# Kernel tuning notes

Hardware: AMD Instinct MI355X
Metric: run time of the kernel (lower is better)

## Reference

```python
import jax, jax.numpy as jnp
import numpy as np
import math

B, N, F = 4, 4096, 64
NEG_SLOPE = 0.01


def _leaky_relu(x):
    return jnp.where(x >= 0, x, NEG_SLOPE * x)


def setup_inputs() -> dict:
    key = jax.random.key(0)
    k1, k2, k3, k4, k5 = jax.random.split(key, 5)
    Q = jax.random.normal(k1, (B, N, F, 2), dtype=jnp.float32)
    K = jax.random.normal(k2, (B, N, F, 2), dtype=jnp.float32)
    V = jax.random.normal(k3, (B, N, F, 2), dtype=jnp.float32)
    W_att = jax.random.normal(k4, (F, F), dtype=jnp.float32) / math.sqrt(F)
    b_att = jax.random.normal(k5, (F,), dtype=jnp.float32) * 0.01
    return {"Q": Q, "K": K, "V": V, "W_att": W_att, "b_att": b_att}


def reference(Q, K, V, W_att, b_att):
    # Split complex components: last axis is (real, imag)
    Qr, Qi = Q[..., 0], Q[..., 1]
    Kr, Ki = K[..., 0], K[..., 1]
    Vr, Vi = V[..., 0], V[..., 1]

    n = Q.shape[1]
    scale = 1.0 / math.sqrt(n)  # num_nodes == N

    # Complex scores = Q @ K^T (no conjugation, as in torch einsum on complex)
    sr = (jnp.einsum('bik,bjk->bij', Qr, Kr) - jnp.einsum('bik,bjk->bij', Qi, Ki)) * scale
    si = (jnp.einsum('bik,bjk->bij', Qr, Ki) + jnp.einsum('bik,bjk->bij', Qi, Kr)) * scale

    # Causal mask: positions j > i are masked out (contribute zero weight)
    causal = jnp.tril(jnp.ones((n, n), dtype=bool))  # [N, N], True = keep
    wr = jnp.where(causal, _leaky_relu(sr), 0.0)
    wi = jnp.where(causal, _leaky_relu(si), 0.0)

    # Attention-weighted values (real weights with real V, imag with imag V)
    out_r = jnp.einsum('bij,bjf->bif', wr, Vr)
    out_i = jnp.einsum('bij,bjf->bif', wi, Vi)

    # att_map: shared linear layer
    out_r = out_r @ W_att.T + b_att
    out_i = out_i @ W_att.T + b_att

    return jnp.stack([out_r, out_i], axis=-1)  # [B, N, F, 2]
```

## Files before the change

### kernel.cpp

```cpp
#include <hip/hip_runtime.h>

#define NB 4
#define NN 4096
#define NF 64
#define TSTEP 8
#define BLKS_PER_B 260

typedef __attribute__((ext_vector_type(8))) short bf16x8;
typedef __attribute__((ext_vector_type(4))) float f32x4;

union S8 { unsigned short u[8]; bf16x8 v; };

__device__ __forceinline__ unsigned short f2bf(float x) {
    unsigned int uu = __builtin_bit_cast(unsigned int, x);
    uu += 0x7fffu + ((uu >> 16) & 1u);
    return (unsigned short)(uu >> 16);
}

__global__ __launch_bounds__(256)
void prep_all(const float* __restrict__ Q, const float* __restrict__ K,
              const float* __restrict__ V, const float* __restrict__ W,
              const float* __restrict__ batt,
              short* __restrict__ QF, short* __restrict__ KF,
              short* __restrict__ VF, short* __restrict__ WF,
              float* __restrict__ out) {
    int tid = blockIdx.x * 256 + threadIdx.x;

    if (tid < 262144) {
        int sel = tid >> 17;
        int r   = tid & 0x1FFFF;
        int l  = r & 63;
        int c  = (r >> 6) & 1;
        int rg = (r >> 7) & 255;
        int b  = r >> 15;
        const float* src = sel ? K : Q;
        short*       dst = sel ? KF : QF;
        float sc = sel ? 1.0f : 0.015625f;

        int row = rg * 16 + (l & 15);
        int k0  = c * 32 + (l >> 4) * 8;
        const float4* s4 = (const float4*)src;
        int base4 = (b * NN + row) * 32 + (k0 >> 1);

        S8 ar, ai;
        #pragma unroll
        for (int m = 0; m < 4; ++m) {
            float4 f = s4[base4 + m];
            ar.u[2 * m]     = f2bf(f.x * sc);
            ar.u[2 * m + 1] = f2bf(f.z * sc);
            ai.u[2 * m]     = f2bf(f.y * sc);
            ai.u[2 * m + 1] = f2bf(f.w * sc);
        }
        int cid0 = ((b * 256 + rg) * 2 + c) * 2;
        *(bf16x8*)(dst + (cid0 + 0) * 512 + l * 8) = ar.v;
        *(bf16x8*)(dst + (cid0 + 1) * 512 + l * 8) = ai.v;
    } else if (tid < 393216) {
        int r = tid - 262144;
        int l  = r & 63;
        int c  = (r >> 6) & 1;
        int ft = (r >> 7) & 3;
        int jt = (r >> 9) & 63;
        int b  = (r >> 15) & 3;

        int f  = ft * 16 + (l & 15);
        int jb = jt * 64 + c * 32 + (l >> 4) * 4;
        const float2* s2 = (const float2*)V;

        S8 ar, ai;
        #pragma unroll
        for (int e = 0; e < 8; ++e) {
            int j = jb + (e >> 2) * 16 + (e & 3);
            float2 gg = s2[(b * NN + j) * 64 + f];
            ar.u[e] = f2bf(gg.x);
            ai.u[e] = f2bf(gg.y);
        }
        int cid0 = (((b * 64 + jt) * 4 + ft) * 2 + c) * 2;
        *(bf16x8*)(VF + (cid0 + 0) * 512 + l * 8) = ar.v;
        *(bf16x8*)(VF + (cid0 + 1) * 512 + l * 8) = ai.v;
    } else if (tid < 393728) {
        int r = tid - 393216;
        int l  = r & 63;
        int c  = (r >> 6) & 1;
        int gt = r >> 7;
        int grow = gt * 16 + (l & 15);
        const float* sp = W + grow * 64;
        S8 a;
        #pragma unroll
        for (int e = 0; e < 8; ++e) {
            int f = c * 32 + (e >> 2) * 16 + (l >> 4) * 4 + (e & 3);
            a.u[e] = f2bf(sp[f]);
        }
        *(bf16x8*)(WF + ((gt * 2 + c) * 64 + l) * 8) = a.v;
    } else {
        int r = tid - 393728;
        int g0 = (2 * r) & 63;
        float b0 = batt[g0];
        float b1 = batt[g0 + 1];
        float4 zz = {b0, b0, b1, b1};
        ((float4*)out)[r] = zz;
    }
}

__device__ __forceinline__ int tri_inv(int g) {
    int it = (int)((__builtin_sqrtf(8.0f * (float)g + 1.0f) - 1.0f) * 0.5f);
    while ((it + 1) * (it + 2) / 2 <= g) ++it;
    while (it * (it + 1) / 2 > g) --it;
    return it;
}

__global__ __launch_bounds__(256, 4)
void attn_main(const short* __restrict__ QF, const short* __restrict__ KF,
               const short* __restrict__ VF, const short* __restrict__ WF,
               const float* __restrict__ batt, float* __restrict__ out) {
    int bid = blockIdx.x;
    int b   = bid / BLKS_PER_B;
    int g   = (bid % BLKS_PER_B) * TSTEP;
    int gend = g + TSTEP;

    int w   = threadIdx.x >> 6;
    int l   = threadIdx.x & 63;
    int r16 = l & 15;
    int lb  = l >> 4;

    const f32x4 z = {0.f, 0.f, 0.f, 0.f};

    while (g < gend) {
        int it   = tri_inv(g);
        int base = it * (it + 1) / 2;
        int jt0  = g - base;
        int cnt  = min(gend - g, it + 1 - jt0);
        int jt1  = jt0 + cnt;

        bf16x8 qf[2][2];
        {
            int rgq = it * 4 + w;
            #pragma unroll
            for (int c = 0; c < 2; ++c)
                #pragma unroll
                for (int ch = 0; ch < 2; ++ch)
                    qf[c][ch] = *(const bf16x8*)(QF + (((b * 256 + rgq) * 2 + c) * 2 + ch) * 512 + l * 8);
        }

        f32x4 o[4][2];
        #pragma unroll
        for (int ft = 0; ft < 4; ++ft) { o[ft][0] = z; o[ft][1] = z; }

        for (int jt = jt0; jt < jt1; ++jt) {
            bool diag = (jt == it);
            bf16x8 pa0r, pa0i, pa1r, pa1i;

            #pragma unroll
            for (int ct = 0; ct < 4; ++ct) {
                bf16x8 kf[2][2];
                int rg = jt * 4 + ct;
                #pragma unroll
                for (int c = 0; c < 2; ++c)
                    #pragma unroll
                    for (int ch = 0; ch < 2; ++ch)
                        kf[c][ch] = *(const bf16x8*)(KF + (((b * 256 + rg) * 2 + c) * 2 + ch) * 512 + l * 8);

                f32x4 t1 = __builtin_amdgcn_mfma_f32_16x16x32_bf16(kf[0][0], qf[0][0], z, 0, 0, 0);
                t1 = __builtin_amdgcn_mfma_f32_16x16x32_bf16(kf[1][0], qf[1][0], t1, 0, 0, 0);
                f32x4 t2 = __builtin_amdgcn_mfma_f32_16x16x32_bf16(kf[0][1], qf[0][1], z, 0, 0, 0);
                t2 = __builtin_amdgcn_mfma_f32_16x16x32_bf16(kf[1][1], qf[1][1], t2, 0, 0, 0);
                f32x4 si = __builtin_amdgcn_mfma_f32_16x16x32_bf16(kf[0][1], qf[0][0], z, 0, 0, 0);
                si = __builtin_amdgcn_mfma_f32_16x16x32_bf16(kf[1][1], qf[1][0], si, 0, 0, 0);
                si = __builtin_amdgcn_mfma_f32_16x16x32_bf16(kf[0][0], qf[0][1], si, 0, 0, 0);
                si = __builtin_amdgcn_mfma_f32_16x16x32_bf16(kf[1][0], qf[1][1], si, 0, 0, 0);

                #pragma unroll
                for (int reg = 0; reg < 4; ++reg) {
                    float sr = t1[reg] - t2[reg];
                    float sv = si[reg];
                    float wr = fmaxf(sr, 0.f) + 0.01f * fminf(sr, 0.f);
                    float wi = fmaxf(sv, 0.f) + 0.01f * fminf(sv, 0.f);
                    if (diag) {
                        int jg = ct * 16 + lb * 4 + reg;
                        int ig = w * 16 + r16;
                        if (jg > ig) { wr = 0.f; wi = 0.f; }
                    }
                    short hr = (short)f2bf(wr);
                    short hi = (short)f2bf(wi);
                    int e = (ct & 1) * 4 + reg;
                    if (ct < 2) { pa0r[e] = hr; pa0i[e] = hi; }
                    else        { pa1r[e] = hr; pa1i[e] = hi; }
                }
            }

            #pragma unroll
            for (int ft = 0; ft < 4; ++ft) {
                int cid0 = (((b * 64 + jt) * 4 + ft) * 2 + 0) * 2;
                bf16x8 v0r = *(const bf16x8*)(VF + (cid0 + 0) * 512 + l * 8);
                bf16x8 v0i = *(const bf16x8*)(VF + (cid0 + 1) * 512 + l * 8);
                bf16x8 v1r = *(const bf16x8*)(VF + (cid0 + 2) * 512 + l * 8);
                bf16x8 v1i = *(const bf16x8*)(VF + (cid0 + 3) * 512 + l * 8);
                o[ft][0] = __builtin_amdgcn_mfma_f32_16x16x32_bf16(v0r, pa0r, o[ft][0], 0, 0, 0);
                o[ft][0] = __builtin_amdgcn_mfma_f32_16x16x32_bf16(v1r, pa1r, o[ft][0], 0, 0, 0);
                o[ft][1] = __builtin_amdgcn_mfma_f32_16x16x32_bf16(v0i, pa0i, o[ft][1], 0, 0, 0);
                o[ft][1] = __builtin_amdgcn_mfma_f32_16x16x32_bf16(v1i, pa1i, o[ft][1], 0, 0, 0);
            }
        }

        bf16x8 ob[2][2];
        #pragma unroll
        for (int cc = 0; cc < 2; ++cc)
            #pragma unroll
            for (int ch = 0; ch < 2; ++ch)
                #pragma unroll
                for (int s = 0; s < 2; ++s)
                    #pragma unroll
                    for (int reg = 0; reg < 4; ++reg)
                        ob[cc][ch][s * 4 + reg] = (short)f2bf(o[cc * 2 + s][ch][reg]);

        bool whole = (jt0 == 0) && (jt1 == it + 1);
        int i0 = it * 64 + w * 16;

        #pragma unroll
        for (int gt = 0; gt < 4; ++gt) {
            bf16x8 wa0 = *(const bf16x8*)(WF + ((gt * 2 + 0) * 64 + l) * 8);
            bf16x8 wa1 = *(const bf16x8*)(WF + ((gt * 2 + 1) * 64 + l) * 8);

            f32x4 a0 = __builtin_amdgcn_mfma_f32_16x16x32_bf16(ob[0][0], wa0, z, 0, 0, 0);
            a0 = __builtin_amdgcn_mfma_f32_16x16x32_bf16(ob[1][0], wa1, a0, 0, 0, 0);
            f32x4 a1 = __builtin_amdgcn_mfma_f32_16x16x32_bf16(ob[0][1], wa0, z, 0, 0, 0);
            a1 = __builtin_amdgcn_mfma_f32_16x16x32_bf16(ob[1][1], wa1, a1, 0, 0, 0);

            int gcol = gt * 16 + r16;
            if (whole) {
                float bb = batt[gcol];
                #pragma unroll
                for (int reg = 0; reg < 4; ++reg) {
                    int irow = i0 + lb * 4 + reg;
                    float2 st = {a0[reg] + bb, a1[reg] + bb};
                    *(float2*)(out + ((b * NN + irow) * 64 + gcol) * 2) = st;
                }
            } else {
                #pragma unroll
                for (int reg = 0; reg < 4; ++reg) {
                    int irow = i0 + lb * 4 + reg;
                    int idx = ((b * NN + irow) * 64 + gcol) * 2;
                    atomicAdd(out + idx,     a0[reg]);
                    atomicAdd(out + idx + 1, a1[reg]);
                }
            }
        }

        g += cnt;
    }
}

extern "C" void kernel_launch(void* const* d_in, const int* in_sizes, int n_in,
                              void* d_out, int out_size, void* d_ws, size_t ws_size,
                              hipStream_t stream) {
    const float* Q  = (const float*)d_in[0];
    const float* K  = (const float*)d_in[1];
    const float* V  = (const float*)d_in[2];
    const float* W  = (const float*)d_in[3];
    const float* bA = (const float*)d_in[4];
    float* out = (float*)d_out;

    short* QF = (short*)d_ws;
    short* KF = QF + 2097152;
    short* VF = KF + 2097152;
    short* WF = VF + 2097152;

    prep_all<<<3586, 256, 0, stream>>>(Q, K, V, W, bA, QF, KF, VF, WF, out);
    attn_main<<<NB * BLKS_PER_B, 256, 0, stream>>>(QF, KF, VF, WF, bA, out);
}
```

Measured before the change: 185.7 us.

## Halve work chunk per block, hoist V loads, split diagonal tile via template

Halves the number of tiles per block (TSTEP 8→4, doubling the grid) and lowers the launch-bounds occupancy hint from 4 to 3 blocks to allow more registers. The tile body becomes a templated helper that issues all V fragment loads before the score MFMAs, so V latency overlaps the QK compute. The diagonal causal-mask branch is split off at compile time, and leaky ReLU plus the bf16 conversions use cheaper forms via the library bf16 intrinsic. Smaller chunks add more partial-tile bias/atomic output handling, and more registers may reduce occupancy.

```diff
diff --git a/kernel.cpp b/kernel.cpp
--- a/kernel.cpp
+++ b/kernel.cpp
@@ -1,10 +1,11 @@
 #include <hip/hip_runtime.h>
+#include <hip/hip_bf16.h>
 
 #define NB 4
 #define NN 4096
 #define NF 64
-#define TSTEP 8
-#define BLKS_PER_B 260
+#define TSTEP 4
+#define BLKS_PER_B 520
 
 typedef __attribute__((ext_vector_type(8))) short bf16x8;
 typedef __attribute__((ext_vector_type(4))) float f32x4;
@@ -15,6 +16,10 @@
     unsigned int uu = __builtin_bit_cast(unsigned int, x);
     uu += 0x7fffu + ((uu >> 16) & 1u);
     return (unsigned short)(uu >> 16);
+}
+
+__device__ __forceinline__ short f2bf_s(float x) {
+    return __builtin_bit_cast(short, __float2bfloat16(x));
 }
 
 __global__ __launch_bounds__(256)
@@ -108,7 +113,73 @@
     return it;
 }
 
-__global__ __launch_bounds__(256, 4)
+template<bool DIAG>
+__device__ __forceinline__ void do_tile(int b, int it, int jt, int w, int l,
+                                        int r16, int lb,
+                                        const bf16x8 (&qf)[2][2], f32x4 (&o)[4][2],
+                                        const short* __restrict__ KF,
+                                        const short* __restrict__ VF) {
+    const f32x4 z = {0.f, 0.f, 0.f, 0.f};
+
+    bf16x8 vf_[4][4];
+    #pragma unroll
+    for (int ft = 0; ft < 4; ++ft) {
+        int cid0 = (((b * 64 + jt) * 4 + ft) * 2) * 2;
+        #pragma unroll
+        for (int q = 0; q < 4; ++q)
+            vf_[ft][q] = *(const bf16x8*)(VF + (cid0 + q) * 512 + l * 8);
+    }
+
+    bf16x8 pa0r, pa0i, pa1r, pa1i;
+
+    #pragma unroll
+    for (int ct = 0; ct < 4; ++ct) {
+        bf16x8 kf[2][2];
+        int rg = jt * 4 + ct;
+        #pragma unroll
+        for (int c = 0; c < 2; ++c)
+            #pragma unroll
+            for (int ch = 0; ch < 2; ++ch)
+                kf[c][ch] = *(const bf16x8*)(KF + (((b * 256 + rg) * 2 + c) * 2 + ch) * 512 + l * 8);
+
+        f32x4 t1 = __builtin_amdgcn_mfma_f32_16x16x32_bf16(kf[0][0], qf[0][0], z, 0, 0, 0);
+        t1 = __builtin_amdgcn_mfma_f32_16x16x32_bf16(kf[1][0], qf[1][0], t1, 0, 0, 0);
+        f32x4 t2 = __builtin_amdgcn_mfma_f32_16x16x32_bf16(kf[0][1], qf[0][1], z, 0, 0, 0);
+        t2 = __builtin_amdgcn_mfma_f32_16x16x32_bf16(kf[1][1], qf[1][1], t2, 0, 0, 0);
+        f32x4 si = __builtin_amdgcn_mfma_f32_16x16x32_bf16(kf[0][1], qf[0][0], z, 0, 0, 0);
+        si = __builtin_amdgcn_mfma_f32_16x16x32_bf16(kf[1][1], qf[1][0], si, 0, 0, 0);
+        si = __builtin_amdgcn_mfma_f32_16x16x32_bf16(kf[0][0], qf[0][1], si, 0, 0, 0);
+        si = __builtin_amdgcn_mfma_f32_16x16x32_bf16(kf[1][0], qf[1][1], si, 0, 0, 0);
+
+        #pragma unroll
+        for (int reg = 0; reg < 4; ++reg) {
+            float sr = t1[reg] - t2[reg];
+            float sv = si[reg];
+            float wr = sr * (sr >= 0.f ? 1.0f : 0.01f);
+            float wi = sv * (sv >= 0.f ? 1.0f : 0.01f);
+            if constexpr (DIAG) {
+                int jg = ct * 16 + lb * 4 + reg;
+                int ig = w * 16 + r16;
+                if (jg > ig) { wr = 0.f; wi = 0.f; }
+            }
+            short hr = f2bf_s(wr);
+            short hi = f2bf_s(wi);
+            int e = (ct & 1) * 4 + reg;
+            if (ct < 2) { pa0r[e] = hr; pa0i[e] = hi; }
+            else        { pa1r[e] = hr; pa1i[e] = hi; }
+        }
+    }
+
+    #pragma unroll
+    for (int ft = 0; ft < 4; ++ft) {
+        o[ft][0] = __builtin_amdgcn_mfma_f32_16x16x32_bf16(vf_[ft][0], pa0r, o[ft][0], 0, 0, 0);
+        o[ft][0] = __builtin_amdgcn_mfma_f32_16x16x32_bf16(vf_[ft][2], pa1r, o[ft][0], 0, 0, 0);
+        o[ft][1] = __builtin_amdgcn_mfma_f32_16x16x32_bf16(vf_[ft][1], pa0i, o[ft][1], 0, 0, 0);
+        o[ft][1] = __builtin_amdgcn_mfma_f32_16x16x32_bf16(vf_[ft][3], pa1i, o[ft][1], 0, 0, 0);
+    }
+}
+
+__global__ __launch_bounds__(256, 3)
 void attn_main(const short* __restrict__ QF, const short* __restrict__ KF,
                const short* __restrict__ VF, const short* __restrict__ WF,
                const float* __restrict__ batt, float* __restrict__ out) {
@@ -145,61 +216,12 @@
         #pragma unroll
         for (int ft = 0; ft < 4; ++ft) { o[ft][0] = z; o[ft][1] = z; }
 
-        for (int jt = jt0; jt < jt1; ++jt) {
-            bool diag = (jt == it);
-            bf16x8 pa0r, pa0i, pa1r, pa1i;
-
-            #pragma unroll
-            for (int ct = 0; ct < 4; ++ct) {
-                bf16x8 kf[2][2];
-                int rg = jt * 4 + ct;
-                #pragma unroll
-                for (int c = 0; c < 2; ++c)
-                    #pragma unroll
-                    for (int ch = 0; ch < 2; ++ch)
-                        kf[c][ch] = *(const bf16x8*)(KF + (((b * 256 + rg) * 2 + c) * 2 + ch) * 512 + l * 8);
-
-                f32x4 t1 = __builtin_amdgcn_mfma_f32_16x16x32_bf16(kf[0][0], qf[0][0], z, 0, 0, 0);
-                t1 = __builtin_amdgcn_mfma_f32_16x16x32_bf16(kf[1][0], qf[1][0], t1, 0, 0, 0);
-                f32x4 t2 = __builtin_amdgcn_mfma_f32_16x16x32_bf16(kf[0][1], qf[0][1], z, 0, 0, 0);
-                t2 = __builtin_amdgcn_mfma_f32_16x16x32_bf16(kf[1][1], qf[1][1], t2, 0, 0, 0);
-                f32x4 si = __builtin_amdgcn_mfma_f32_16x16x32_bf16(kf[0][1], qf[0][0], z, 0, 0, 0);
-                si = __builtin_amdgcn_mfma_f32_16x16x32_bf16(kf[1][1], qf[1][0], si, 0, 0, 0);
-                si = __builtin_amdgcn_mfma_f32_16x16x32_bf16(kf[0][0], qf[0][1], si, 0, 0, 0);
-                si = __builtin_amdgcn_mfma_f32_16x16x32_bf16(kf[1][0], qf[1][1], si, 0, 0, 0);
-
-                #pragma unroll
-                for (int reg = 0; reg < 4; ++reg) {
-                    float sr = t1[reg] - t2[reg];
-                    float sv = si[reg];
-                    float wr = fmaxf(sr, 0.f) + 0.01f * fminf(sr, 0.f);
-                    float wi = fmaxf(sv, 0.f) + 0.01f * fminf(sv, 0.f);
-                    if (diag) {
-                        int jg = ct * 16 + lb * 4 + reg;
-                        int ig = w * 16 + r16;
-                        if (jg > ig) { wr = 0.f; wi = 0.f; }
-                    }
-                    short hr = (short)f2bf(wr);
-                    short hi = (short)f2bf(wi);
-                    int e = (ct & 1) * 4 + reg;
-                    if (ct < 2) { pa0r[e] = hr; pa0i[e] = hi; }
-                    else        { pa1r[e] = hr; pa1i[e] = hi; }
-                }
-            }
-
-            #pragma unroll
-            for (int ft = 0; ft < 4; ++ft) {
-                int cid0 = (((b * 64 + jt) * 4 + ft) * 2 + 0) * 2;
-                bf16x8 v0r = *(const bf16x8*)(VF + (cid0 + 0) * 512 + l * 8);
-                bf16x8 v0i = *(const bf16x8*)(VF + (cid0 + 1) * 512 + l * 8);
-                bf16x8 v1r = *(const bf16x8*)(VF + (cid0 + 2) * 512 + l * 8);
-                bf16x8 v1i = *(const bf16x8*)(VF + (cid0 + 3) * 512 + l * 8);
-                o[ft][0] = __builtin_amdgcn_mfma_f32_16x16x32_bf16(v0r, pa0r, o[ft][0], 0, 0, 0);
-                o[ft][0] = __builtin_amdgcn_mfma_f32_16x16x32_bf16(v1r, pa1r, o[ft][0], 0, 0, 0);
-                o[ft][1] = __builtin_amdgcn_mfma_f32_16x16x32_bf16(v0i, pa0i, o[ft][1], 0, 0, 0);
-                o[ft][1] = __builtin_amdgcn_mfma_f32_16x16x32_bf16(v1i, pa1i, o[ft][1], 0, 0, 0);
-            }
-        }
+        bool hasdiag = (jt1 == it + 1);
+        int nd_end   = hasdiag ? it : jt1;
+        for (int jt = jt0; jt < nd_end; ++jt)
+            do_tile<false>(b, it, jt, w, l, r16, lb, qf, o, KF, VF);
+        if (hasdiag)
+            do_tile<true>(b, it, it, w, l, r16, lb, qf, o, KF, VF);
 
         bf16x8 ob[2][2];
         #pragma unroll
@@ -210,7 +232,7 @@
                 for (int s = 0; s < 2; ++s)
                     #pragma unroll
                     for (int reg = 0; reg < 4; ++reg)
-                        ob[cc][ch][s * 4 + reg] = (short)f2bf(o[cc * 2 + s][ch][reg]);
+                        ob[cc][ch][s * 4 + reg] = f2bf_s(o[cc * 2 + s][ch][reg]);
 
         bool whole = (jt0 == 0) && (jt1 == it + 1);
         int i0 = it * 64 + w * 16;
```

Measured after the change: 216.9 us. 1.17x slower.
